# Optimization experiments

Hardware: AMD Instinct MI355X
Metric: run time of the kernel (lower is better)

The kernel has to match this reference:

```python
import jax, jax.numpy as jnp
import numpy as np
from jax import lax

DIM = 512
HEADS = 8
HEAD_DIM = DIM // HEADS
FS = 56            # features_size -> H = W = 56
SR = 2             # sr_ratio
N = FS * FS        # query tokens = 3136
KN = (FS // SR) ** 2  # kv tokens = 784
B = 4
SCALE = HEAD_DIM ** -0.5
LN_EPS = 1e-5


def _relative_indices(fs):
    # matches generate_relative_distance: [[x, y] for x in range(fs) for y in range(fs)]
    coords = np.stack(np.meshgrid(np.arange(fs), np.arange(fs), indexing='ij'), -1).reshape(-1, 2)
    dist = coords[None, :, :] - coords[:, None, :] + (fs - 1)   # (N, N, 2), values in [0, 2fs-2]
    return jnp.asarray(dist, dtype=jnp.int32)


def setup_inputs() -> dict:
    key = jax.random.key(0)
    ks = jax.random.split(key, 8)
    s = 0.02
    return {
        'x':    jax.random.normal(ks[0], (B, DIM, FS, FS), jnp.float32),
        'Wq':   jax.random.normal(ks[1], (DIM, DIM), jnp.float32) * s,
        'Wkv':  jax.random.normal(ks[2], (DIM, 2 * DIM), jnp.float32) * s,
        'Wsr':  jax.random.normal(ks[3], (DIM, DIM, SR, SR), jnp.float32) * s,  # OIHW
        'b_sr': jnp.zeros((DIM,), jnp.float32),
        'gamma': jnp.ones((DIM,), jnp.float32),
        'beta':  jnp.zeros((DIM,), jnp.float32),
        'Wp':   jax.random.normal(ks[4], (DIM, DIM), jnp.float32) * s,
        'bp':   jnp.zeros((DIM,), jnp.float32),
        'pos':  jax.random.normal(ks[5], (2 * FS - 1, 2 * FS - 1), jnp.float32) * 0.2,
        'rel_idx': _relative_indices(FS),
    }


def reference(x, Wq, Wkv, Wsr, b_sr, gamma, beta, Wp, bp, pos, rel_idx):
    b, c, h, w = x.shape
    n = h * w
    xq = x.reshape(b, c, n).transpose(0, 2, 1)                      # B N C
    q = (xq @ Wq).reshape(b, n, HEADS, HEAD_DIM).transpose(0, 2, 1, 3)  # B h N d

    # spatial reduction of k/v: Conv2d(k=SR, s=SR) + LayerNorm
    xr = lax.conv_general_dilated(x, Wsr, (SR, SR), 'VALID',
                                  dimension_numbers=('NCHW', 'OIHW', 'NCHW'))
    xr = xr + b_sr[None, :, None, None]
    kn = xr.shape[2] * xr.shape[3]
    xkv = xr.reshape(b, c, kn).transpose(0, 2, 1)                   # B KN C
    mu = xkv.mean(-1, keepdims=True)
    var = ((xkv - mu) ** 2).mean(-1, keepdims=True)
    xkv = (xkv - mu) * lax.rsqrt(var + LN_EPS) * gamma + beta

    # kv projection; rearrange 'B N (dim h l) -> l B h N dim'
    kv = (xkv @ Wkv).reshape(b, kn, HEAD_DIM, HEADS, 2)
    k = kv[..., 0].transpose(0, 3, 1, 2)                            # B h KN d
    v = kv[..., 1].transpose(0, 3, 1, 2)                            # B h KN d

    attn = jnp.einsum('bhnd,bhmd->bhnm', q, k) * SCALE              # B h N KN
    bias = pos[rel_idx[:, :kn, 0], rel_idx[:, :kn, 1]]              # N KN gathered bias
    attn = jax.nn.softmax(attn + bias, axis=-1)

    out = jnp.einsum('bhnm,bhmd->bhnd', attn, v)                    # B h N d
    out = out.transpose(0, 2, 1, 3).reshape(b, n, c)                # B N C
    out = out @ Wp + bp
    return out.transpose(0, 2, 1).reshape(b, c, h, w)
```

## Files before the change

kernel.cpp:

```cpp
#include <hip/hip_runtime.h>
#include <hip/hip_bf16.h>
#include <cstdint>

constexpr int BATCH = 4;
constexpr int CDIM  = 512;
constexpr int NHEAD = 8;
constexpr int HD    = 64;
constexpr int FSP   = 56;
constexpr int NTOK  = FSP * FSP;
constexpr int KH    = 28;
constexpr int KNTOK = KH * KH;
constexpr float SCALE_ATT = 0.125f;
constexpr int BIAS_LD = 832;

typedef _Float16 f16;
typedef __attribute__((ext_vector_type(8))) _Float16 half8;
typedef __attribute__((ext_vector_type(4))) float  floatx4;

__device__ __forceinline__ void tr64(const float* __restrict__ in,
                                     f16* __restrict__ out, int R, int C,
                                     int r0, int c0, float (*sm)[65], int tid) {
  const int rr = tid >> 2, cs = (tid & 3) * 16;
  const float* src = in + (size_t)(r0 + rr) * C + c0 + cs;
#pragma unroll
  for (int j = 0; j < 16; j += 4) *(float4*)&sm[rr][cs + j] = *(const float4*)&src[j];
  __syncthreads();
  f16* dh = out + (size_t)(c0 + rr) * R + r0 + cs;
  half8 v0, v1;
#pragma unroll
  for (int j = 0; j < 8; ++j) v0[j] = (f16)sm[cs + j][rr];
#pragma unroll
  for (int j = 0; j < 8; ++j) v1[j] = (f16)sm[cs + 8 + j][rr];
  *(half8*)&dh[0] = v0;
  *(half8*)&dh[8] = v1;
}

__global__ __launch_bounds__(256) void k_prep(const float* __restrict__ x,
                                              const float* __restrict__ Wq,
                                              const float* __restrict__ Wkv,
                                              const float* __restrict__ Wp,
                                              const float* __restrict__ Wsr,
                                              const float* __restrict__ pos,
                                              f16* __restrict__ xT,
                                              f16* __restrict__ WqT,
                                              f16* __restrict__ WkvT,
                                              f16* __restrict__ WpT,
                                              f16* __restrict__ WsrP,
                                              float* __restrict__ biasT) {
  __shared__ float sm[64][65];
  const int tid = threadIdx.x;
  int bid = blockIdx.x;
  if (bid < 1568) {
    const int b = bid / 392, r = bid % 392;
    tr64(x + (size_t)b * CDIM * NTOK, xT + (size_t)b * NTOK * CDIM,
         CDIM, NTOK, (r % 8) * 64, (r / 8) * 64, sm, tid);
    return;
  }
  bid -= 1568;
  if (bid < 64)  { tr64(Wq,  WqT,  512, 512,  (bid % 8) * 64, (bid / 8) * 64, sm, tid); return; }
  bid -= 64;
  if (bid < 128) { tr64(Wkv, WkvT, 512, 1024, (bid % 8) * 64, (bid / 8) * 64, sm, tid); return; }
  bid -= 128;
  if (bid < 64)  { tr64(Wp,  WpT,  512, 512,  (bid % 8) * 64, (bid / 8) * 64, sm, tid); return; }
  bid -= 64;
  if (bid < 512) {
    const float* src = Wsr + (size_t)bid * 2048;
    f16* dh = WsrP + (size_t)bid * 2048;
    for (int kp = tid; kp < 2048; kp += 256) {
      const int dd = kp >> 9, c = kp & 511;
      dh[kp] = (f16)src[c * 4 + dd];
    }
    return;
  }
  bid -= 512;
  {
    const int n = bid;
    const int in_ = n / FSP, jn = n % FSP;
    const int cbase = 55 * 111 + 55 - in_ * 111 - jn;
    for (int i = tid; i < BIAS_LD; i += 256) {
      const int jc = i >> 6, w = i & 63, txx = w >> 2, tt = w & 3;
      const int m = jc * 64 + tt * 16 + txx;
      float v = -30000.f;
      if (m < KNTOK) {
        const int im = m / FSP, jm = m % FSP;
        v = pos[cbase + im * 111 + jm];
      }
      biasT[(size_t)n * BIAS_LD + i] = v;
    }
  }
}

struct GemmSmem { f16 A[128 * 32]; f16 B[128 * 32]; };

__device__ __forceinline__ void gl_lds(const f16* g, f16* l) {
  __builtin_amdgcn_global_load_lds(
      (const __attribute__((address_space(1))) void*)g,
      (__attribute__((address_space(3))) void*)l, 16, 0, 0);
}

__device__ __forceinline__ void gemm128(GemmSmem* sm,
    const f16* a0, const f16* a1, const f16* b0, const f16* b1,
    int lane, int wv, int wm, int wn, int quad, int tx,
    floatx4 acc[4][4]) {
  f16* lA0 = sm->A + wv * 1024 + lane * 8;
  f16* lA1 = sm->A + wv * 1024 + 512 + lane * 8;
  f16* lB0 = sm->B + wv * 1024 + lane * 8;
  f16* lB1 = sm->B + wv * 1024 + 512 + lane * 8;
  for (int it = 0; it < 16; ++it) {
    gl_lds(a0 + it * 32, lA0);
    gl_lds(a1 + it * 32, lA1);
    gl_lds(b0 + it * 32, lB0);
    gl_lds(b1 + it * 32, lB1);
    __syncthreads();
    half8 af[4], bf[4];
#pragma unroll
    for (int i = 0; i < 4; ++i)
      af[i] = *(const half8*)&sm->A[(wm * 64 + i * 16 + tx) * 32 + quad * 8];
#pragma unroll
    for (int j = 0; j < 4; ++j)
      bf[j] = *(const half8*)&sm->B[(wn * 64 + j * 16 + tx) * 32 + quad * 8];
#pragma unroll
    for (int j = 0; j < 4; ++j)
#pragma unroll
      for (int i = 0; i < 4; ++i)
        acc[i][j] = __builtin_amdgcn_mfma_f32_16x16x32_f16(af[i], bf[j], acc[i][j], 0, 0, 0);
    __syncthreads();
  }
}

#define GEMM128_PRE()                                                     \
  const int tid = threadIdx.x, lane = tid & 63, wv = tid >> 6;            \
  const int wm = wv & 1, wn = wv >> 1, quad = lane >> 4, tx = lane & 15;  \
  const int lr = lane >> 2, lc = (lane & 3) * 8;                          \
  floatx4 acc[4][4];                                                      \
  _Pragma("unroll") for (int i = 0; i < 4; ++i)                           \
  _Pragma("unroll") for (int j = 0; j < 4; ++j)                           \
      acc[i][j] = (floatx4){0.f, 0.f, 0.f, 0.f};

__global__ __launch_bounds__(256) void k_gemmA(const f16* __restrict__ xT,
                                               const f16* __restrict__ WqT,
                                               f16* __restrict__ Qh,
                                               const f16* __restrict__ WsrP,
                                               float* __restrict__ XRp) {
  __shared__ GemmSmem sm;
  GEMM128_PRE();
  int bid = blockIdx.x;
  if (bid < 400) {
    const int b = bid / 100, t = bid % 100;
    const int m0 = (t >> 2) * 128, n0 = (t & 3) * 128;
    const f16* xb = xT + (size_t)b * NTOK * CDIM;
    const int r0 = wv * 32 + lr, r1 = r0 + 16;
    const f16* a0 = xb + (size_t)min(m0 + r0, NTOK - 1) * CDIM + lc;
    const f16* a1 = xb + (size_t)min(m0 + r1, NTOK - 1) * CDIM + lc;
    const f16* b0 = WqT + (size_t)(n0 + r0) * CDIM + lc;
    const f16* b1 = WqT + (size_t)(n0 + r1) * CDIM + lc;
    gemm128(&sm, a0, a1, b0, b1, lane, wv, wm, wn, quad, tx, acc);
    f16* qhB = Qh + (size_t)b * NTOK * CDIM;
#pragma unroll
    for (int i = 0; i < 4; ++i)
#pragma unroll
      for (int rg = 0; rg < 4; ++rg) {
        const int m = m0 + wm * 64 + i * 16 + quad * 4 + rg;
        if (m >= NTOK) continue;
#pragma unroll
        for (int j = 0; j < 4; ++j)
          qhB[(size_t)m * CDIM + n0 + wn * 64 + j * 16 + tx] = (f16)acc[i][j][rg];
      }
  } else {
    bid -= 400;
    const int bkc = bid / 28, r = bid % 28;
    const int b = bkc >> 2, kc = bkc & 3;
    const int m0 = (r >> 2) * 128, n0 = (r & 3) * 128;
    const f16* xb = xT + (size_t)b * NTOK * CDIM;
    const int r0 = wv * 32 + lr, r1 = r0 + 16;
    int am0 = m0 + r0; if (am0 >= KNTOK) am0 = 0;
    int am1 = m0 + r1; if (am1 >= KNTOK) am1 = 0;
    const int sp0 = 112 * (am0 / KH) + 2 * (am0 % KH) + (kc >> 1) * FSP + (kc & 1);
    const int sp1 = 112 * (am1 / KH) + 2 * (am1 % KH) + (kc >> 1) * FSP + (kc & 1);
    const f16* a0 = xb + (size_t)sp0 * CDIM + lc;
    const f16* a1 = xb + (size_t)sp1 * CDIM + lc;
    const f16* b0 = WsrP + (size_t)(n0 + r0) * 2048 + kc * 512 + lc;
    const f16* b1 = WsrP + (size_t)(n0 + r1) * 2048 + kc * 512 + lc;
    gemm128(&sm, a0, a1, b0, b1, lane, wv, wm, wn, quad, tx, acc);
    float* dst = XRp + (size_t)(kc * BATCH + b) * KNTOK * CDIM;
#pragma unroll
    for (int i = 0; i < 4; ++i)
#pragma unroll
      for (int rg = 0; rg < 4; ++rg) {
        const int m = m0 + wm * 64 + i * 16 + quad * 4 + rg;
        if (m >= KNTOK) continue;
#pragma unroll
        for (int j = 0; j < 4; ++j)
          dst[(size_t)m * CDIM + n0 + wn * 64 + j * 16 + tx] = acc[i][j][rg];
      }
  }
}

__global__ __launch_bounds__(256) void k_ln(const float* __restrict__ XRp,
                                            const float* __restrict__ b_sr,
                                            const float* __restrict__ gamma,
                                            const float* __restrict__ beta,
                                            f16* __restrict__ oh) {
  const int row = blockIdx.x;
  const size_t slab = (size_t)BATCH * KNTOK * CDIM;
  const float* p = XRp + (size_t)row * CDIM;
  const int tid = threadIdx.x;
  const float v0 = p[tid] + p[tid + slab] + p[tid + 2 * slab] + p[tid + 3 * slab]
                 + b_sr[tid];
  const float v1 = p[tid + 256] + p[tid + 256 + slab] + p[tid + 256 + 2 * slab]
                 + p[tid + 256 + 3 * slab] + b_sr[tid + 256];
  float s = v0 + v1;
  float s2 = v0 * v0 + v1 * v1;
#pragma unroll
  for (int mask = 32; mask >= 1; mask >>= 1) {
    s  += __shfl_xor(s, mask, 64);
    s2 += __shfl_xor(s2, mask, 64);
  }
  __shared__ float ws[4], ws2[4];
  const int wid = tid >> 6;
  if ((tid & 63) == 0) { ws[wid] = s; ws2[wid] = s2; }
  __syncthreads();
  const float ts  = ws[0] + ws[1] + ws[2] + ws[3];
  const float ts2 = ws2[0] + ws2[1] + ws2[2] + ws2[3];
  const float mu  = ts * (1.f / CDIM);
  const float var = ts2 * (1.f / CDIM) - mu * mu;
  const float rs  = rsqrtf(var + 1e-5f);
  const size_t base = (size_t)row * CDIM;
  oh[base + tid]       = (f16)((v0 - mu) * rs * gamma[tid] + beta[tid]);
  oh[base + tid + 256] = (f16)((v1 - mu) * rs * gamma[tid + 256] + beta[tid + 256]);
}

__global__ __launch_bounds__(256) void k_kvproj(const f16* __restrict__ XRh,
                                                const f16* __restrict__ WkvT,
                                                f16* __restrict__ Kh,
                                                f16* __restrict__ Vt) {
  __shared__ GemmSmem sm;
  GEMM128_PRE();
  const int bid = blockIdx.x;
  const int b = bid / 56, r = bid % 56;
  const int m0 = (r / 8) * 128, n0 = (r % 8) * 128;
  const f16* ab = XRh + (size_t)b * KNTOK * CDIM;
  const int r0 = wv * 32 + lr, r1 = r0 + 16;
  const f16* a0 = ab + (size_t)min(m0 + r0, KNTOK - 1) * CDIM + lc;
  const f16* a1 = ab + (size_t)min(m0 + r1, KNTOK - 1) * CDIM + lc;
  const f16* b0 = WkvT + (size_t)(n0 + r0) * CDIM + lc;
  const f16* b1 = WkvT + (size_t)(n0 + r1) * CDIM + lc;
  gemm128(&sm, a0, a1, b0, b1, lane, wv, wm, wn, quad, tx, acc);
#pragma unroll
  for (int i = 0; i < 4; ++i)
#pragma unroll
    for (int rg = 0; rg < 4; ++rg) {
      const int m = m0 + wm * 64 + i * 16 + quad * 4 + rg;
      if (m >= KNTOK) continue;
#pragma unroll
      for (int j = 0; j < 4; ++j) {
        const int o2 = n0 + wn * 64 + j * 16 + tx;
        const int d = o2 >> 4, hh = (o2 >> 1) & 7;
        const float v = acc[i][j][rg];
        if (o2 & 1)
          Vt[((size_t)(b * NHEAD + hh) * HD + d) * KNTOK + m] = (f16)v;
        else
          Kh[((size_t)(b * NHEAD + hh) * KNTOK + m) * HD + d] = (f16)v;
      }
    }
}

#define LSTR 72
__global__ __launch_bounds__(256) void k_attn(const f16* __restrict__ Qh,
                                              const f16* __restrict__ Kh,
                                              const f16* __restrict__ Vt,
                                              const float* __restrict__ biasT,
                                              f16* __restrict__ Oh) {
  __shared__ f16 Qhs[128][LSTR], Khs[64][LSTR], Vts[64][LSTR];
  __shared__ f16 Ps[4][32][LSTR];
  const int b = blockIdx.x >> 3, h = blockIdx.x & 7;
  const int n0 = blockIdx.y * 128;
  const int tid = threadIdx.x, lane = tid & 63, wv = tid >> 6;
  const int quad = lane >> 4, tx = lane & 15;
  const int rr = tid >> 2, sg = (tid & 3) * 16;
  const int qr = tid >> 1, qs = (tid & 1) * 32;

  const f16* khB = Kh + (size_t)(b * NHEAD + h) * KNTOK * HD;
  const f16* vtB = Vt + (size_t)(b * NHEAD + h) * HD * KNTOK;

  {
    const int qrow = min(n0 + qr, NTOK - 1);
    const f16* src = Qh + ((size_t)b * NTOK + qrow) * CDIM + h * HD + qs;
    *(half8*)&Qhs[qr][qs]      = *(const half8*)&src[0];
    *(half8*)&Qhs[qr][qs + 8]  = *(const half8*)&src[8];
    *(half8*)&Qhs[qr][qs + 16] = *(const half8*)&src[16];
    *(half8*)&Qhs[qr][qs + 24] = *(const half8*)&src[24];
    const size_t koff = (size_t)rr * HD + sg;
    *(half8*)&Khs[rr][sg]     = *(const half8*)&khB[koff];
    *(half8*)&Khs[rr][sg + 8] = *(const half8*)&khB[koff + 8];
    const size_t voff = (size_t)rr * KNTOK + sg;
    *(half8*)&Vts[rr][sg]     = *(const half8*)&vtB[voff];
    *(half8*)&Vts[rr][sg + 8] = *(const half8*)&vtB[voff + 8];
  }

  size_t bbase[2][4];
#pragma unroll
  for (int i = 0; i < 2; ++i)
#pragma unroll
    for (int rg = 0; rg < 4; ++rg) {
      const int grow = min(n0 + wv * 32 + i * 16 + quad * 4 + rg, NTOK - 1);
      bbase[i][rg] = (size_t)grow * BIAS_LD + tx * 4;
    }

  floatx4 acc_o[2][4];
#pragma unroll
  for (int i = 0; i < 2; ++i)
#pragma unroll
    for (int t = 0; t < 4; ++t) acc_o[i][t] = (floatx4){0.f, 0.f, 0.f, 0.f};
  float l_part[2][4] = {};
  __syncthreads();

  half8 nk0, nk1, nv0, nv1;
  for (int jc = 0; jc < 13; ++jc) {
    if (jc < 12) {
      const int mbn = (jc + 1) * 64;
      const int km = min(mbn + rr, KNTOK - 1);
      const size_t koff = (size_t)km * HD + sg;
      nk0 = *(const half8*)&khB[koff];
      nk1 = *(const half8*)&khB[koff + 8];
      const int vc = min(mbn + sg, KNTOK - 16);
      const size_t voff = (size_t)rr * KNTOK + vc;
      nv0 = *(const half8*)&vtB[voff];
      nv1 = *(const half8*)&vtB[voff + 8];
    }

    floatx4 sc[2][4];
#pragma unroll
    for (int i = 0; i < 2; ++i)
#pragma unroll
      for (int t = 0; t < 4; ++t) sc[i][t] = (floatx4){0.f, 0.f, 0.f, 0.f};
#pragma unroll
    for (int ks = 0; ks < 2; ++ks) {
      const int kk = ks * 32 + quad * 8;
      half8 aq[2];
#pragma unroll
      for (int i = 0; i < 2; ++i)
        aq[i] = *(const half8*)&Qhs[wv * 32 + i * 16 + tx][kk];
#pragma unroll
      for (int t = 0; t < 4; ++t) {
        const half8 bk = *(const half8*)&Khs[t * 16 + tx][kk];
#pragma unroll
        for (int i = 0; i < 2; ++i)
          sc[i][t] = __builtin_amdgcn_mfma_f32_16x16x32_f16(aq[i], bk, sc[i][t], 0, 0, 0);
      }
    }

#pragma unroll
    for (int i = 0; i < 2; ++i)
#pragma unroll
      for (int rg = 0; rg < 4; ++rg) {
        const float4 bb = *(const float4*)&biasT[bbase[i][rg] + jc * 64];
        const float p0 = __expf(fmaf(sc[i][0][rg], SCALE_ATT, bb.x));
        const float p1 = __expf(fmaf(sc[i][1][rg], SCALE_ATT, bb.y));
        const float p2 = __expf(fmaf(sc[i][2][rg], SCALE_ATT, bb.z));
        const float p3 = __expf(fmaf(sc[i][3][rg], SCALE_ATT, bb.w));
        l_part[i][rg] += (p0 + p1) + (p2 + p3);
        const int prow = i * 16 + quad * 4 + rg;
        Ps[wv][prow][0 * 16 + tx] = (f16)p0;
        Ps[wv][prow][1 * 16 + tx] = (f16)p1;
        Ps[wv][prow][2 * 16 + tx] = (f16)p2;
        Ps[wv][prow][3 * 16 + tx] = (f16)p3;
      }

#pragma unroll
    for (int ks = 0; ks < 2; ++ks) {
      const int kk = ks * 32 + quad * 8;
      half8 ap[2];
#pragma unroll
      for (int i = 0; i < 2; ++i)
        ap[i] = *(const half8*)&Ps[wv][i * 16 + tx][kk];
#pragma unroll
      for (int t = 0; t < 4; ++t) {
        const half8 bv = *(const half8*)&Vts[t * 16 + tx][kk];
#pragma unroll
        for (int i = 0; i < 2; ++i)
          acc_o[i][t] = __builtin_amdgcn_mfma_f32_16x16x32_f16(ap[i], bv, acc_o[i][t], 0, 0, 0);
      }
    }
    __syncthreads();
    if (jc < 12) {
      *(half8*)&Khs[rr][sg]     = nk0;
      *(half8*)&Khs[rr][sg + 8] = nk1;
      *(half8*)&Vts[rr][sg]     = nv0;
      *(half8*)&Vts[rr][sg + 8] = nv1;
    }
    __syncthreads();
  }

#pragma unroll
  for (int i = 0; i < 2; ++i)
#pragma unroll
    for (int rg = 0; rg < 4; ++rg) {
      float l = l_part[i][rg];
#pragma unroll
      for (int msk = 1; msk < 16; msk <<= 1) l += __shfl_xor(l, msk, 64);
      const float inv = 1.f / l;
      const int grow = n0 + wv * 32 + i * 16 + quad * 4 + rg;
      if (grow < NTOK) {
        const size_t base = ((size_t)b * NTOK + grow) * CDIM + h * HD;
#pragma unroll
        for (int t = 0; t < 4; ++t)
          Oh[base + t * 16 + tx] = (f16)(acc_o[i][t][rg] * inv);
      }
    }
}

__global__ __launch_bounds__(256) void k_outproj(const f16* __restrict__ Og,
                                                 const f16* __restrict__ WpT,
                                                 const float* __restrict__ bp,
                                                 float* __restrict__ out) {
  __shared__ GemmSmem sm;
  GEMM128_PRE();
  const int bid = blockIdx.x;
  const int b = bid / 100, t = bid % 100;
  const int m0 = (t >> 2) * 128, n0 = (t & 3) * 128;
  const f16* ab = Og + (size_t)b * NTOK * CDIM;
  const int r0 = wv * 32 + lr, r1 = r0 + 16;
  const f16* a0 = ab + (size_t)min(m0 + r0, NTOK - 1) * CDIM + lc;
  const f16* a1 = ab + (size_t)min(m0 + r1, NTOK - 1) * CDIM + lc;
  const f16* b0 = WpT + (size_t)(n0 + r0) * CDIM + lc;
  const f16* b1 = WpT + (size_t)(n0 + r1) * CDIM + lc;
  gemm128(&sm, a0, a1, b0, b1, lane, wv, wm, wn, quad, tx, acc);
#pragma unroll
  for (int j = 0; j < 4; ++j) {
    const int co = n0 + wn * 64 + j * 16 + tx;
    const float bpv = bp[co];
    float* obase = out + ((size_t)b * CDIM + co) * NTOK;
#pragma unroll
    for (int i = 0; i < 4; ++i) {
      const int mb4 = m0 + wm * 64 + i * 16 + quad * 4;
      if (mb4 < NTOK) {
        floatx4 v = acc[i][j] + bpv;
        *(floatx4*)&obase[mb4] = v;
      }
    }
  }
}

extern "C" void kernel_launch(void* const* d_in, const int* in_sizes, int n_in,
                              void* d_out, int out_size, void* d_ws, size_t ws_size,
                              hipStream_t stream) {
  const float* x     = (const float*)d_in[0];
  const float* Wq    = (const float*)d_in[1];
  const float* Wkv   = (const float*)d_in[2];
  const float* Wsr   = (const float*)d_in[3];
  const float* b_sr  = (const float*)d_in[4];
  const float* gamma = (const float*)d_in[5];
  const float* beta  = (const float*)d_in[6];
  const float* Wp    = (const float*)d_in[7];
  const float* bp    = (const float*)d_in[8];
  const float* pos   = (const float*)d_in[9];
  float* out = (float*)d_out;

  char* p = (char*)d_ws;
  auto alloc = [&](size_t bytes) -> void* {
    void* r = (void*)p;
    p += (bytes + 255) & ~(size_t)255;
    return r;
  };
  const size_t SZ_BNC = (size_t)BATCH * NTOK * CDIM;
  const size_t SZ_BKC = (size_t)BATCH * KNTOK * CDIM;
  const size_t SZ_KV  = (size_t)BATCH * NHEAD * KNTOK * HD;

  f16* xT    = (f16*)alloc(SZ_BNC * 2);
  f16* WqT   = (f16*)alloc(512 * 512 * 2);
  f16* WkvT  = (f16*)alloc(1024 * 512 * 2);
  f16* WpT   = (f16*)alloc(512 * 512 * 2);
  f16* WsrP  = (f16*)alloc(512 * 2048 * 2);
  f16* Qh    = (f16*)alloc(SZ_BNC * 2);
  float* XRp = (float*)alloc(SZ_BKC * 4 * 4);
  f16* XRh   = (f16*)alloc(SZ_BKC * 2);
  f16* Vt    = (f16*)alloc(SZ_KV * 2);
  float* biasT = (float*)alloc((size_t)NTOK * BIAS_LD * 4);

  f16* Kh = (f16*)XRp;
  f16* Og = xT;

  const dim3 blk(256);
  k_prep   <<<dim3(5472), blk, 0, stream>>>(x, Wq, Wkv, Wp, Wsr, pos,
                                            xT, WqT, WkvT, WpT, WsrP, biasT);
  k_gemmA  <<<dim3(848),  blk, 0, stream>>>(xT, WqT, Qh, WsrP, XRp);
  k_ln     <<<dim3(BATCH * KNTOK), blk, 0, stream>>>(XRp, b_sr, gamma, beta, XRh);
  k_kvproj <<<dim3(224),  blk, 0, stream>>>(XRh, WkvT, Kh, Vt);
  k_attn   <<<dim3(BATCH * NHEAD, 25), blk, 0, stream>>>(Qh, Kh, Vt, biasT, Og);
  k_outproj<<<dim3(400),  blk, 0, stream>>>(Og, WpT, bp, out);
}
```

Before: 284.6 us.

## Fuse Q projection into attention kernel and halve SR-conv split-K partials

The Q projection GEMM moves out of the standalone GEMM kernel into the attention kernel. Each block computes its 128x64 Q tile from xT and WqT in shared memory before the attention loop, so the Qh buffer round trip through global memory goes away. The SR convolution now runs as its own kernel and accumulates two kernel positions per block, which halves the fp32 partial slabs that LayerNorm must read and sum. In exchange, each attention block repeats part of the Q GEMM work with a small 32-wide K step, and the SR conv launches fewer, longer blocks.

```diff
diff --git a/kernel.cpp b/kernel.cpp
--- a/kernel.cpp
+++ b/kernel.cpp
@@ -137,63 +137,43 @@
   _Pragma("unroll") for (int j = 0; j < 4; ++j)                           \
       acc[i][j] = (floatx4){0.f, 0.f, 0.f, 0.f};
 
-__global__ __launch_bounds__(256) void k_gemmA(const f16* __restrict__ xT,
-                                               const f16* __restrict__ WqT,
-                                               f16* __restrict__ Qh,
-                                               const f16* __restrict__ WsrP,
-                                               float* __restrict__ XRp) {
+__global__ __launch_bounds__(256) void k_srconv(const f16* __restrict__ xT,
+                                                const f16* __restrict__ WsrP,
+                                                float* __restrict__ XRp) {
   __shared__ GemmSmem sm;
   GEMM128_PRE();
-  int bid = blockIdx.x;
-  if (bid < 400) {
-    const int b = bid / 100, t = bid % 100;
-    const int m0 = (t >> 2) * 128, n0 = (t & 3) * 128;
-    const f16* xb = xT + (size_t)b * NTOK * CDIM;
-    const int r0 = wv * 32 + lr, r1 = r0 + 16;
-    const f16* a0 = xb + (size_t)min(m0 + r0, NTOK - 1) * CDIM + lc;
-    const f16* a1 = xb + (size_t)min(m0 + r1, NTOK - 1) * CDIM + lc;
-    const f16* b0 = WqT + (size_t)(n0 + r0) * CDIM + lc;
-    const f16* b1 = WqT + (size_t)(n0 + r1) * CDIM + lc;
-    gemm128(&sm, a0, a1, b0, b1, lane, wv, wm, wn, quad, tx, acc);
-    f16* qhB = Qh + (size_t)b * NTOK * CDIM;
-#pragma unroll
-    for (int i = 0; i < 4; ++i)
-#pragma unroll
-      for (int rg = 0; rg < 4; ++rg) {
-        const int m = m0 + wm * 64 + i * 16 + quad * 4 + rg;
-        if (m >= NTOK) continue;
-#pragma unroll
-        for (int j = 0; j < 4; ++j)
-          qhB[(size_t)m * CDIM + n0 + wn * 64 + j * 16 + tx] = (f16)acc[i][j][rg];
-      }
-  } else {
-    bid -= 400;
-    const int bkc = bid / 28, r = bid % 28;
-    const int b = bkc >> 2, kc = bkc & 3;
-    const int m0 = (r >> 2) * 128, n0 = (r & 3) * 128;
-    const f16* xb = xT + (size_t)b * NTOK * CDIM;
-    const int r0 = wv * 32 + lr, r1 = r0 + 16;
-    int am0 = m0 + r0; if (am0 >= KNTOK) am0 = 0;
-    int am1 = m0 + r1; if (am1 >= KNTOK) am1 = 0;
-    const int sp0 = 112 * (am0 / KH) + 2 * (am0 % KH) + (kc >> 1) * FSP + (kc & 1);
-    const int sp1 = 112 * (am1 / KH) + 2 * (am1 % KH) + (kc >> 1) * FSP + (kc & 1);
+  const int bid = blockIdx.x;
+  const int bkc = bid / 28, r = bid % 28;
+  const int b = bkc >> 1, kc2 = bkc & 1;
+  const int m0 = (r >> 2) * 128, n0 = (r & 3) * 128;
+  const f16* xb = xT + (size_t)b * NTOK * CDIM;
+  const int r0 = wv * 32 + lr, r1 = r0 + 16;
+  int am0 = m0 + r0; if (am0 >= KNTOK) am0 = 0;
+  int am1 = m0 + r1; if (am1 >= KNTOK) am1 = 0;
+  const int base0 = 112 * (am0 / KH) + 2 * (am0 % KH);
+  const int base1 = 112 * (am1 / KH) + 2 * (am1 % KH);
+#pragma unroll
+  for (int dd2 = 0; dd2 < 2; ++dd2) {
+    const int dd = kc2 * 2 + dd2;
+    const int sp0 = base0 + (dd >> 1) * FSP + (dd & 1);
+    const int sp1 = base1 + (dd >> 1) * FSP + (dd & 1);
     const f16* a0 = xb + (size_t)sp0 * CDIM + lc;
     const f16* a1 = xb + (size_t)sp1 * CDIM + lc;
-    const f16* b0 = WsrP + (size_t)(n0 + r0) * 2048 + kc * 512 + lc;
-    const f16* b1 = WsrP + (size_t)(n0 + r1) * 2048 + kc * 512 + lc;
+    const f16* b0 = WsrP + (size_t)(n0 + r0) * 2048 + dd * 512 + lc;
+    const f16* b1 = WsrP + (size_t)(n0 + r1) * 2048 + dd * 512 + lc;
     gemm128(&sm, a0, a1, b0, b1, lane, wv, wm, wn, quad, tx, acc);
-    float* dst = XRp + (size_t)(kc * BATCH + b) * KNTOK * CDIM;
-#pragma unroll
-    for (int i = 0; i < 4; ++i)
-#pragma unroll
-      for (int rg = 0; rg < 4; ++rg) {
-        const int m = m0 + wm * 64 + i * 16 + quad * 4 + rg;
-        if (m >= KNTOK) continue;
-#pragma unroll
-        for (int j = 0; j < 4; ++j)
-          dst[(size_t)m * CDIM + n0 + wn * 64 + j * 16 + tx] = acc[i][j][rg];
-      }
-  }
+  }
+  float* dst = XRp + (size_t)(kc2 * BATCH + b) * KNTOK * CDIM;
+#pragma unroll
+  for (int i = 0; i < 4; ++i)
+#pragma unroll
+    for (int rg = 0; rg < 4; ++rg) {
+      const int m = m0 + wm * 64 + i * 16 + quad * 4 + rg;
+      if (m >= KNTOK) continue;
+#pragma unroll
+      for (int j = 0; j < 4; ++j)
+        dst[(size_t)m * CDIM + n0 + wn * 64 + j * 16 + tx] = acc[i][j][rg];
+    }
 }
 
 __global__ __launch_bounds__(256) void k_ln(const float* __restrict__ XRp,
@@ -205,10 +185,8 @@
   const size_t slab = (size_t)BATCH * KNTOK * CDIM;
   const float* p = XRp + (size_t)row * CDIM;
   const int tid = threadIdx.x;
-  const float v0 = p[tid] + p[tid + slab] + p[tid + 2 * slab] + p[tid + 3 * slab]
-                 + b_sr[tid];
-  const float v1 = p[tid + 256] + p[tid + 256 + slab] + p[tid + 256 + 2 * slab]
-                 + p[tid + 256 + 3 * slab] + b_sr[tid + 256];
+  const float v0 = p[tid] + p[tid + slab] + b_sr[tid];
+  const float v1 = p[tid + 256] + p[tid + 256 + slab] + b_sr[tid + 256];
   float s = v0 + v1;
   float s2 = v0 * v0 + v1 * v1;
 #pragma unroll
@@ -266,7 +244,9 @@
 }
 
 #define LSTR 72
-__global__ __launch_bounds__(256) void k_attn(const f16* __restrict__ Qh,
+#define GSTR 40
+__global__ __launch_bounds__(256) void k_attn(const f16* __restrict__ xT,
+                                              const f16* __restrict__ WqT,
                                               const f16* __restrict__ Kh,
                                               const f16* __restrict__ Vt,
                                               const float* __restrict__ biasT,
@@ -278,18 +258,13 @@
   const int tid = threadIdx.x, lane = tid & 63, wv = tid >> 6;
   const int quad = lane >> 4, tx = lane & 15;
   const int rr = tid >> 2, sg = (tid & 3) * 16;
-  const int qr = tid >> 1, qs = (tid & 1) * 32;
-
+
+  const f16* xb  = xT + (size_t)b * NTOK * CDIM;
+  const f16* wq  = WqT + (size_t)(h * HD) * CDIM;
   const f16* khB = Kh + (size_t)(b * NHEAD + h) * KNTOK * HD;
   const f16* vtB = Vt + (size_t)(b * NHEAD + h) * HD * KNTOK;
 
   {
-    const int qrow = min(n0 + qr, NTOK - 1);
-    const f16* src = Qh + ((size_t)b * NTOK + qrow) * CDIM + h * HD + qs;
-    *(half8*)&Qhs[qr][qs]      = *(const half8*)&src[0];
-    *(half8*)&Qhs[qr][qs + 8]  = *(const half8*)&src[8];
-    *(half8*)&Qhs[qr][qs + 16] = *(const half8*)&src[16];
-    *(half8*)&Qhs[qr][qs + 24] = *(const half8*)&src[24];
     const size_t koff = (size_t)rr * HD + sg;
     *(half8*)&Khs[rr][sg]     = *(const half8*)&khB[koff];
     *(half8*)&Khs[rr][sg + 8] = *(const half8*)&khB[koff + 8];
@@ -298,6 +273,53 @@
     *(half8*)&Vts[rr][sg + 8] = *(const half8*)&vtB[voff + 8];
   }
 
+  {
+    f16* Astage = &Qhs[0][0];
+    f16* Bstage = &Ps[0][0][0];
+    const int ar = tid >> 1, as_ = (tid & 1) * 16;
+    const int br = tid >> 2, bs_ = (tid & 3) * 8;
+    const f16* aP = xb + (size_t)min(n0 + ar, NTOK - 1) * CDIM + as_;
+    const f16* bP = wq + (size_t)br * CDIM + bs_;
+    floatx4 qacc[2][4];
+#pragma unroll
+    for (int i = 0; i < 2; ++i)
+#pragma unroll
+      for (int j = 0; j < 4; ++j) qacc[i][j] = (floatx4){0.f, 0.f, 0.f, 0.f};
+    half8 ra0 = *(const half8*)&aP[0], ra1 = *(const half8*)&aP[8];
+    half8 rb0 = *(const half8*)&bP[0];
+    for (int it = 0; it < 16; ++it) {
+      *(half8*)&Astage[ar * GSTR + as_]     = ra0;
+      *(half8*)&Astage[ar * GSTR + as_ + 8] = ra1;
+      *(half8*)&Bstage[br * GSTR + bs_]     = rb0;
+      __syncthreads();
+      if (it + 1 < 16) {
+        const f16* an = aP + (it + 1) * 32;
+        const f16* bn = bP + (it + 1) * 32;
+        ra0 = *(const half8*)&an[0]; ra1 = *(const half8*)&an[8];
+        rb0 = *(const half8*)&bn[0];
+      }
+      half8 af[2];
+#pragma unroll
+      for (int i = 0; i < 2; ++i)
+        af[i] = *(const half8*)&Astage[(wv * 32 + i * 16 + tx) * GSTR + quad * 8];
+#pragma unroll
+      for (int j = 0; j < 4; ++j) {
+        const half8 bf = *(const half8*)&Bstage[(j * 16 + tx) * GSTR + quad * 8];
+#pragma unroll
+        for (int i = 0; i < 2; ++i)
+          qacc[i][j] = __builtin_amdgcn_mfma_f32_16x16x32_f16(af[i], bf, qacc[i][j], 0, 0, 0);
+      }
+      __syncthreads();
+    }
+#pragma unroll
+    for (int i = 0; i < 2; ++i)
+#pragma unroll
+      for (int j = 0; j < 4; ++j)
+#pragma unroll
+        for (int rg = 0; rg < 4; ++rg)
+          Qhs[wv * 32 + i * 16 + quad * 4 + rg][j * 16 + tx] = (f16)qacc[i][j][rg];
+  }
+
   size_t bbase[2][4];
 #pragma unroll
   for (int i = 0; i < 2; ++i)
@@ -313,7 +335,6 @@
 #pragma unroll
     for (int t = 0; t < 4; ++t) acc_o[i][t] = (floatx4){0.f, 0.f, 0.f, 0.f};
   float l_part[2][4] = {};
-  __syncthreads();
 
   half8 nk0, nk1, nv0, nv1;
   for (int jc = 0; jc < 13; ++jc) {
@@ -472,21 +493,20 @@
   f16* WkvT  = (f16*)alloc(1024 * 512 * 2);
   f16* WpT   = (f16*)alloc(512 * 512 * 2);
   f16* WsrP  = (f16*)alloc(512 * 2048 * 2);
-  f16* Qh    = (f16*)alloc(SZ_BNC * 2);
-  float* XRp = (float*)alloc(SZ_BKC * 4 * 4);
+  float* XRp = (float*)alloc(SZ_BKC * 4 * 2);
   f16* XRh   = (f16*)alloc(SZ_BKC * 2);
   f16* Vt    = (f16*)alloc(SZ_KV * 2);
+  f16* Og    = (f16*)alloc(SZ_BNC * 2);
   float* biasT = (float*)alloc((size_t)NTOK * BIAS_LD * 4);
 
   f16* Kh = (f16*)XRp;
-  f16* Og = xT;
 
   const dim3 blk(256);
   k_prep   <<<dim3(5472), blk, 0, stream>>>(x, Wq, Wkv, Wp, Wsr, pos,
                                             xT, WqT, WkvT, WpT, WsrP, biasT);
-  k_gemmA  <<<dim3(848),  blk, 0, stream>>>(xT, WqT, Qh, WsrP, XRp);
+  k_srconv <<<dim3(224),  blk, 0, stream>>>(xT, WsrP, XRp);
   k_ln     <<<dim3(BATCH * KNTOK), blk, 0, stream>>>(XRp, b_sr, gamma, beta, XRh);
   k_kvproj <<<dim3(224),  blk, 0, stream>>>(XRh, WkvT, Kh, Vt);
-  k_attn   <<<dim3(BATCH * NHEAD, 25), blk, 0, stream>>>(Qh, Kh, Vt, biasT, Og);
+  k_attn   <<<dim3(BATCH * NHEAD, 25), blk, 0, stream>>>(xT, WqT, Kh, Vt, biasT, Og);
   k_outproj<<<dim3(400),  blk, 0, stream>>>(Og, WpT, bp, out);
 }
```

New measurement: 297.0 us. +4.4%, slower.

## Halve conv split-K partials, keep Q fragments in registers, coalesce bias writes

Applied to the files above, without the earlier changes.

The spatial-reduction conv GEMM now runs two of the four kernel taps per block and accumulates them in registers. This halves the fp32 partial buffer and the reads LayerNorm does from it, and cuts the gemmA grid from 848 to 624 blocks. Attention drops the shared Q tile: each wave stages its own Q rows through its P scratch buffer and holds the MFMA fragments in registers, which lowers LDS use and repeated LDS reads. The bias prep loop now reads pos contiguously and scatters the writes. Fewer split-K blocks may reduce parallelism, and keeping Q in registers raises register pressure.

```diff
diff --git a/kernel.cpp b/kernel.cpp
--- a/kernel.cpp
+++ b/kernel.cpp
@@ -77,15 +77,12 @@
     const int n = bid;
     const int in_ = n / FSP, jn = n % FSP;
     const int cbase = 55 * 111 + 55 - in_ * 111 - jn;
-    for (int i = tid; i < BIAS_LD; i += 256) {
-      const int jc = i >> 6, w = i & 63, txx = w >> 2, tt = w & 3;
-      const int m = jc * 64 + tt * 16 + txx;
+    float* dst = biasT + (size_t)n * BIAS_LD;
+    for (int m = tid; m < BIAS_LD; m += 256) {
       float v = -30000.f;
-      if (m < KNTOK) {
-        const int im = m / FSP, jm = m % FSP;
-        v = pos[cbase + im * 111 + jm];
-      }
-      biasT[(size_t)n * BIAS_LD + i] = v;
+      if (m < KNTOK) v = pos[cbase + (m / FSP) * 111 + (m % FSP)];
+      const int jc = m >> 6, w = m & 63, t = w >> 4, txx = w & 15;
+      dst[jc * 64 + txx * 4 + t] = v;
     }
   }
 }
@@ -169,20 +166,26 @@
   } else {
     bid -= 400;
     const int bkc = bid / 28, r = bid % 28;
-    const int b = bkc >> 2, kc = bkc & 3;
+    const int b = bkc >> 1, kc2 = bkc & 1;
     const int m0 = (r >> 2) * 128, n0 = (r & 3) * 128;
     const f16* xb = xT + (size_t)b * NTOK * CDIM;
     const int r0 = wv * 32 + lr, r1 = r0 + 16;
     int am0 = m0 + r0; if (am0 >= KNTOK) am0 = 0;
     int am1 = m0 + r1; if (am1 >= KNTOK) am1 = 0;
-    const int sp0 = 112 * (am0 / KH) + 2 * (am0 % KH) + (kc >> 1) * FSP + (kc & 1);
-    const int sp1 = 112 * (am1 / KH) + 2 * (am1 % KH) + (kc >> 1) * FSP + (kc & 1);
-    const f16* a0 = xb + (size_t)sp0 * CDIM + lc;
-    const f16* a1 = xb + (size_t)sp1 * CDIM + lc;
-    const f16* b0 = WsrP + (size_t)(n0 + r0) * 2048 + kc * 512 + lc;
-    const f16* b1 = WsrP + (size_t)(n0 + r1) * 2048 + kc * 512 + lc;
-    gemm128(&sm, a0, a1, b0, b1, lane, wv, wm, wn, quad, tx, acc);
-    float* dst = XRp + (size_t)(kc * BATCH + b) * KNTOK * CDIM;
+    const int base0 = 112 * (am0 / KH) + 2 * (am0 % KH);
+    const int base1 = 112 * (am1 / KH) + 2 * (am1 % KH);
+#pragma unroll
+    for (int dd2 = 0; dd2 < 2; ++dd2) {
+      const int dd = kc2 * 2 + dd2;
+      const int sp0 = base0 + (dd >> 1) * FSP + (dd & 1);
+      const int sp1 = base1 + (dd >> 1) * FSP + (dd & 1);
+      const f16* a0 = xb + (size_t)sp0 * CDIM + lc;
+      const f16* a1 = xb + (size_t)sp1 * CDIM + lc;
+      const f16* b0 = WsrP + (size_t)(n0 + r0) * 2048 + dd * 512 + lc;
+      const f16* b1 = WsrP + (size_t)(n0 + r1) * 2048 + dd * 512 + lc;
+      gemm128(&sm, a0, a1, b0, b1, lane, wv, wm, wn, quad, tx, acc);
+    }
+    float* dst = XRp + (size_t)(kc2 * BATCH + b) * KNTOK * CDIM;
 #pragma unroll
     for (int i = 0; i < 4; ++i)
 #pragma unroll
@@ -205,10 +208,8 @@
   const size_t slab = (size_t)BATCH * KNTOK * CDIM;
   const float* p = XRp + (size_t)row * CDIM;
   const int tid = threadIdx.x;
-  const float v0 = p[tid] + p[tid + slab] + p[tid + 2 * slab] + p[tid + 3 * slab]
-                 + b_sr[tid];
-  const float v1 = p[tid + 256] + p[tid + 256 + slab] + p[tid + 256 + 2 * slab]
-                 + p[tid + 256 + 3 * slab] + b_sr[tid + 256];
+  const float v0 = p[tid] + p[tid + slab] + b_sr[tid];
+  const float v1 = p[tid + 256] + p[tid + 256 + slab] + b_sr[tid + 256];
   float s = v0 + v1;
   float s2 = v0 * v0 + v1 * v1;
 #pragma unroll
@@ -271,31 +272,41 @@
                                               const f16* __restrict__ Vt,
                                               const float* __restrict__ biasT,
                                               f16* __restrict__ Oh) {
-  __shared__ f16 Qhs[128][LSTR], Khs[64][LSTR], Vts[64][LSTR];
+  __shared__ f16 Khs[64][LSTR], Vts[64][LSTR];
   __shared__ f16 Ps[4][32][LSTR];
   const int b = blockIdx.x >> 3, h = blockIdx.x & 7;
   const int n0 = blockIdx.y * 128;
   const int tid = threadIdx.x, lane = tid & 63, wv = tid >> 6;
   const int quad = lane >> 4, tx = lane & 15;
   const int rr = tid >> 2, sg = (tid & 3) * 16;
-  const int qr = tid >> 1, qs = (tid & 1) * 32;
 
   const f16* khB = Kh + (size_t)(b * NHEAD + h) * KNTOK * HD;
   const f16* vtB = Vt + (size_t)(b * NHEAD + h) * HD * KNTOK;
+  f16* PsW = &Ps[wv][0][0];
 
   {
-    const int qrow = min(n0 + qr, NTOK - 1);
-    const f16* src = Qh + ((size_t)b * NTOK + qrow) * CDIM + h * HD + qs;
-    *(half8*)&Qhs[qr][qs]      = *(const half8*)&src[0];
-    *(half8*)&Qhs[qr][qs + 8]  = *(const half8*)&src[8];
-    *(half8*)&Qhs[qr][qs + 16] = *(const half8*)&src[16];
-    *(half8*)&Qhs[qr][qs + 24] = *(const half8*)&src[24];
     const size_t koff = (size_t)rr * HD + sg;
     *(half8*)&Khs[rr][sg]     = *(const half8*)&khB[koff];
     *(half8*)&Khs[rr][sg + 8] = *(const half8*)&khB[koff + 8];
     const size_t voff = (size_t)rr * KNTOK + sg;
     *(half8*)&Vts[rr][sg]     = *(const half8*)&vtB[voff];
     *(half8*)&Vts[rr][sg + 8] = *(const half8*)&vtB[voff + 8];
+  }
+
+  half8 qreg[2][2];
+  {
+    const int qr2 = lane >> 1, qs2 = (lane & 1) * 32;
+    const int qrow = min(n0 + wv * 32 + qr2, NTOK - 1);
+    const f16* src = Qh + ((size_t)b * NTOK + qrow) * CDIM + h * HD + qs2;
+    *(half8*)&PsW[qr2 * LSTR + qs2]      = *(const half8*)&src[0];
+    *(half8*)&PsW[qr2 * LSTR + qs2 + 8]  = *(const half8*)&src[8];
+    *(half8*)&PsW[qr2 * LSTR + qs2 + 16] = *(const half8*)&src[16];
+    *(half8*)&PsW[qr2 * LSTR + qs2 + 24] = *(const half8*)&src[24];
+#pragma unroll
+    for (int i = 0; i < 2; ++i)
+#pragma unroll
+      for (int ks = 0; ks < 2; ++ks)
+        qreg[i][ks] = *(const half8*)&PsW[(i * 16 + tx) * LSTR + ks * 32 + quad * 8];
   }
 
   size_t bbase[2][4];
@@ -337,16 +348,12 @@
 #pragma unroll
     for (int ks = 0; ks < 2; ++ks) {
       const int kk = ks * 32 + quad * 8;
-      half8 aq[2];
-#pragma unroll
-      for (int i = 0; i < 2; ++i)
-        aq[i] = *(const half8*)&Qhs[wv * 32 + i * 16 + tx][kk];
 #pragma unroll
       for (int t = 0; t < 4; ++t) {
         const half8 bk = *(const half8*)&Khs[t * 16 + tx][kk];
 #pragma unroll
         for (int i = 0; i < 2; ++i)
-          sc[i][t] = __builtin_amdgcn_mfma_f32_16x16x32_f16(aq[i], bk, sc[i][t], 0, 0, 0);
+          sc[i][t] = __builtin_amdgcn_mfma_f32_16x16x32_f16(qreg[i][ks], bk, sc[i][t], 0, 0, 0);
       }
     }
 
@@ -361,10 +368,10 @@
         const float p3 = __expf(fmaf(sc[i][3][rg], SCALE_ATT, bb.w));
         l_part[i][rg] += (p0 + p1) + (p2 + p3);
         const int prow = i * 16 + quad * 4 + rg;
-        Ps[wv][prow][0 * 16 + tx] = (f16)p0;
-        Ps[wv][prow][1 * 16 + tx] = (f16)p1;
-        Ps[wv][prow][2 * 16 + tx] = (f16)p2;
-        Ps[wv][prow][3 * 16 + tx] = (f16)p3;
+        PsW[prow * LSTR + 0 * 16 + tx] = (f16)p0;
+        PsW[prow * LSTR + 1 * 16 + tx] = (f16)p1;
+        PsW[prow * LSTR + 2 * 16 + tx] = (f16)p2;
+        PsW[prow * LSTR + 3 * 16 + tx] = (f16)p3;
       }
 
 #pragma unroll
@@ -373,7 +380,7 @@
       half8 ap[2];
 #pragma unroll
       for (int i = 0; i < 2; ++i)
-        ap[i] = *(const half8*)&Ps[wv][i * 16 + tx][kk];
+        ap[i] = *(const half8*)&PsW[(i * 16 + tx) * LSTR + kk];
 #pragma unroll
       for (int t = 0; t < 4; ++t) {
         const half8 bv = *(const half8*)&Vts[t * 16 + tx][kk];
@@ -473,7 +480,7 @@
   f16* WpT   = (f16*)alloc(512 * 512 * 2);
   f16* WsrP  = (f16*)alloc(512 * 2048 * 2);
   f16* Qh    = (f16*)alloc(SZ_BNC * 2);
-  float* XRp = (float*)alloc(SZ_BKC * 4 * 4);
+  float* XRp = (float*)alloc(SZ_BKC * 4 * 2);
   f16* XRh   = (f16*)alloc(SZ_BKC * 2);
   f16* Vt    = (f16*)alloc(SZ_KV * 2);
   float* biasT = (float*)alloc((size_t)NTOK * BIAS_LD * 4);
@@ -484,7 +491,7 @@
   const dim3 blk(256);
   k_prep   <<<dim3(5472), blk, 0, stream>>>(x, Wq, Wkv, Wp, Wsr, pos,
                                             xT, WqT, WkvT, WpT, WsrP, biasT);
-  k_gemmA  <<<dim3(848),  blk, 0, stream>>>(xT, WqT, Qh, WsrP, XRp);
+  k_gemmA  <<<dim3(624),  blk, 0, stream>>>(xT, WqT, Qh, WsrP, XRp);
   k_ln     <<<dim3(BATCH * KNTOK), blk, 0, stream>>>(XRp, b_sr, gamma, beta, XRh);
   k_kvproj <<<dim3(224),  blk, 0, stream>>>(XRh, WkvT, Kh, Vt);
   k_attn   <<<dim3(BATCH * NHEAD, 25), blk, 0, stream>>>(Qh, Kh, Vt, biasT, Og);
```

Result: slower. 327.5 us (+15.1%).

## Move Wkv/Wp transposes and bias table build into the GEMM-A launch

Applied to the files above, without the earlier changes.

The Wkv and Wp transposes and the relative-position bias table construction move out of the prep kernel and run as extra blocks of the Q/spatial-reduction GEMM launch, since only later kernels need them. The idea is to shrink the serial prep kernel and let that independent work fill idle CUs during the GEMM phase. Shared memory becomes a union arena sized for the transpose tile. The bias write pattern is also restructured so global reads of pos are sequential and the permutation happens on the store side, which may make the stores less coalesced.

```diff
diff --git a/kernel.cpp b/kernel.cpp
--- a/kernel.cpp
+++ b/kernel.cpp
@@ -37,16 +37,10 @@
 
 __global__ __launch_bounds__(256) void k_prep(const float* __restrict__ x,
                                               const float* __restrict__ Wq,
-                                              const float* __restrict__ Wkv,
-                                              const float* __restrict__ Wp,
                                               const float* __restrict__ Wsr,
-                                              const float* __restrict__ pos,
                                               f16* __restrict__ xT,
                                               f16* __restrict__ WqT,
-                                              f16* __restrict__ WkvT,
-                                              f16* __restrict__ WpT,
-                                              f16* __restrict__ WsrP,
-                                              float* __restrict__ biasT) {
+                                              f16* __restrict__ WsrP) {
   __shared__ float sm[64][65];
   const int tid = threadIdx.x;
   int bid = blockIdx.x;
@@ -57,35 +51,14 @@
     return;
   }
   bid -= 1568;
-  if (bid < 64)  { tr64(Wq,  WqT,  512, 512,  (bid % 8) * 64, (bid / 8) * 64, sm, tid); return; }
+  if (bid < 64) { tr64(Wq, WqT, 512, 512, (bid % 8) * 64, (bid / 8) * 64, sm, tid); return; }
   bid -= 64;
-  if (bid < 128) { tr64(Wkv, WkvT, 512, 1024, (bid % 8) * 64, (bid / 8) * 64, sm, tid); return; }
-  bid -= 128;
-  if (bid < 64)  { tr64(Wp,  WpT,  512, 512,  (bid % 8) * 64, (bid / 8) * 64, sm, tid); return; }
-  bid -= 64;
-  if (bid < 512) {
+  {
     const float* src = Wsr + (size_t)bid * 2048;
     f16* dh = WsrP + (size_t)bid * 2048;
     for (int kp = tid; kp < 2048; kp += 256) {
       const int dd = kp >> 9, c = kp & 511;
       dh[kp] = (f16)src[c * 4 + dd];
-    }
-    return;
-  }
-  bid -= 512;
-  {
-    const int n = bid;
-    const int in_ = n / FSP, jn = n % FSP;
-    const int cbase = 55 * 111 + 55 - in_ * 111 - jn;
-    for (int i = tid; i < BIAS_LD; i += 256) {
-      const int jc = i >> 6, w = i & 63, txx = w >> 2, tt = w & 3;
-      const int m = jc * 64 + tt * 16 + txx;
-      float v = -30000.f;
-      if (m < KNTOK) {
-        const int im = m / FSP, jm = m % FSP;
-        v = pos[cbase + im * 111 + jm];
-      }
-      biasT[(size_t)n * BIAS_LD + i] = v;
     }
   }
 }
@@ -128,8 +101,8 @@
   }
 }
 
-#define GEMM128_PRE()                                                     \
-  const int tid = threadIdx.x, lane = tid & 63, wv = tid >> 6;            \
+#define GEMM128_VARS()                                                    \
+  const int lane = tid & 63, wv = tid >> 6;                               \
   const int wm = wv & 1, wn = wv >> 1, quad = lane >> 4, tx = lane & 15;  \
   const int lr = lane >> 2, lc = (lane & 3) * 8;                          \
   floatx4 acc[4][4];                                                      \
@@ -141,58 +114,87 @@
                                                const f16* __restrict__ WqT,
                                                f16* __restrict__ Qh,
                                                const f16* __restrict__ WsrP,
-                                               float* __restrict__ XRp) {
-  __shared__ GemmSmem sm;
-  GEMM128_PRE();
+                                               float* __restrict__ XRp,
+                                               const float* __restrict__ Wkv,
+                                               const float* __restrict__ Wp,
+                                               const float* __restrict__ pos,
+                                               f16* __restrict__ WkvT,
+                                               f16* __restrict__ WpT,
+                                               float* __restrict__ biasT) {
+  __shared__ __align__(16) char arena[64 * 65 * 4];
+  GemmSmem* sm = (GemmSmem*)arena;
+  float (*tsm)[65] = (float(*)[65])arena;
+  const int tid = threadIdx.x;
   int bid = blockIdx.x;
-  if (bid < 400) {
-    const int b = bid / 100, t = bid % 100;
-    const int m0 = (t >> 2) * 128, n0 = (t & 3) * 128;
-    const f16* xb = xT + (size_t)b * NTOK * CDIM;
-    const int r0 = wv * 32 + lr, r1 = r0 + 16;
-    const f16* a0 = xb + (size_t)min(m0 + r0, NTOK - 1) * CDIM + lc;
-    const f16* a1 = xb + (size_t)min(m0 + r1, NTOK - 1) * CDIM + lc;
-    const f16* b0 = WqT + (size_t)(n0 + r0) * CDIM + lc;
-    const f16* b1 = WqT + (size_t)(n0 + r1) * CDIM + lc;
-    gemm128(&sm, a0, a1, b0, b1, lane, wv, wm, wn, quad, tx, acc);
-    f16* qhB = Qh + (size_t)b * NTOK * CDIM;
-#pragma unroll
-    for (int i = 0; i < 4; ++i)
-#pragma unroll
-      for (int rg = 0; rg < 4; ++rg) {
-        const int m = m0 + wm * 64 + i * 16 + quad * 4 + rg;
-        if (m >= NTOK) continue;
-#pragma unroll
-        for (int j = 0; j < 4; ++j)
-          qhB[(size_t)m * CDIM + n0 + wn * 64 + j * 16 + tx] = (f16)acc[i][j][rg];
-      }
-  } else {
-    bid -= 400;
-    const int bkc = bid / 28, r = bid % 28;
-    const int b = bkc >> 2, kc = bkc & 3;
-    const int m0 = (r >> 2) * 128, n0 = (r & 3) * 128;
-    const f16* xb = xT + (size_t)b * NTOK * CDIM;
-    const int r0 = wv * 32 + lr, r1 = r0 + 16;
-    int am0 = m0 + r0; if (am0 >= KNTOK) am0 = 0;
-    int am1 = m0 + r1; if (am1 >= KNTOK) am1 = 0;
-    const int sp0 = 112 * (am0 / KH) + 2 * (am0 % KH) + (kc >> 1) * FSP + (kc & 1);
-    const int sp1 = 112 * (am1 / KH) + 2 * (am1 % KH) + (kc >> 1) * FSP + (kc & 1);
-    const f16* a0 = xb + (size_t)sp0 * CDIM + lc;
-    const f16* a1 = xb + (size_t)sp1 * CDIM + lc;
-    const f16* b0 = WsrP + (size_t)(n0 + r0) * 2048 + kc * 512 + lc;
-    const f16* b1 = WsrP + (size_t)(n0 + r1) * 2048 + kc * 512 + lc;
-    gemm128(&sm, a0, a1, b0, b1, lane, wv, wm, wn, quad, tx, acc);
-    float* dst = XRp + (size_t)(kc * BATCH + b) * KNTOK * CDIM;
-#pragma unroll
-    for (int i = 0; i < 4; ++i)
-#pragma unroll
-      for (int rg = 0; rg < 4; ++rg) {
-        const int m = m0 + wm * 64 + i * 16 + quad * 4 + rg;
-        if (m >= KNTOK) continue;
-#pragma unroll
-        for (int j = 0; j < 4; ++j)
-          dst[(size_t)m * CDIM + n0 + wn * 64 + j * 16 + tx] = acc[i][j][rg];
-      }
+  if (bid < 848) {
+    GEMM128_VARS();
+    if (bid < 400) {
+      const int b = bid / 100, t = bid % 100;
+      const int m0 = (t >> 2) * 128, n0 = (t & 3) * 128;
+      const f16* xb = xT + (size_t)b * NTOK * CDIM;
+      const int r0 = wv * 32 + lr, r1 = r0 + 16;
+      const f16* a0 = xb + (size_t)min(m0 + r0, NTOK - 1) * CDIM + lc;
+      const f16* a1 = xb + (size_t)min(m0 + r1, NTOK - 1) * CDIM + lc;
+      const f16* b0 = WqT + (size_t)(n0 + r0) * CDIM + lc;
+      const f16* b1 = WqT + (size_t)(n0 + r1) * CDIM + lc;
+      gemm128(sm, a0, a1, b0, b1, lane, wv, wm, wn, quad, tx, acc);
+      f16* qhB = Qh + (size_t)b * NTOK * CDIM;
+#pragma unroll
+      for (int i = 0; i < 4; ++i)
+#pragma unroll
+        for (int rg = 0; rg < 4; ++rg) {
+          const int m = m0 + wm * 64 + i * 16 + quad * 4 + rg;
+          if (m >= NTOK) continue;
+#pragma unroll
+          for (int j = 0; j < 4; ++j)
+            qhB[(size_t)m * CDIM + n0 + wn * 64 + j * 16 + tx] = (f16)acc[i][j][rg];
+        }
+    } else {
+      bid -= 400;
+      const int bkc = bid / 28, r = bid % 28;
+      const int b = bkc >> 2, kc = bkc & 3;
+      const int m0 = (r >> 2) * 128, n0 = (r & 3) * 128;
+      const f16* xb = xT + (size_t)b * NTOK * CDIM;
+      const int r0 = wv * 32 + lr, r1 = r0 + 16;
+      int am0 = m0 + r0; if (am0 >= KNTOK) am0 = 0;
+      int am1 = m0 + r1; if (am1 >= KNTOK) am1 = 0;
+      const int sp0 = 112 * (am0 / KH) + 2 * (am0 % KH) + (kc >> 1) * FSP + (kc & 1);
+      const int sp1 = 112 * (am1 / KH) + 2 * (am1 % KH) + (kc >> 1) * FSP + (kc & 1);
+      const f16* a0 = xb + (size_t)sp0 * CDIM + lc;
+      const f16* a1 = xb + (size_t)sp1 * CDIM + lc;
+      const f16* b0 = WsrP + (size_t)(n0 + r0) * 2048 + kc * 512 + lc;
+      const f16* b1 = WsrP + (size_t)(n0 + r1) * 2048 + kc * 512 + lc;
+      gemm128(sm, a0, a1, b0, b1, lane, wv, wm, wn, quad, tx, acc);
+      float* dst = XRp + (size_t)(kc * BATCH + b) * KNTOK * CDIM;
+#pragma unroll
+      for (int i = 0; i < 4; ++i)
+#pragma unroll
+        for (int rg = 0; rg < 4; ++rg) {
+          const int m = m0 + wm * 64 + i * 16 + quad * 4 + rg;
+          if (m >= KNTOK) continue;
+#pragma unroll
+          for (int j = 0; j < 4; ++j)
+            dst[(size_t)m * CDIM + n0 + wn * 64 + j * 16 + tx] = acc[i][j][rg];
+        }
+    }
+    return;
+  }
+  bid -= 848;
+  if (bid < 128) { tr64(Wkv, WkvT, 512, 1024, (bid % 8) * 64, (bid / 8) * 64, tsm, tid); return; }
+  bid -= 128;
+  if (bid < 64)  { tr64(Wp,  WpT,  512, 512,  (bid % 8) * 64, (bid / 8) * 64, tsm, tid); return; }
+  bid -= 64;
+  {
+    const int n = bid;
+    const int in_ = n / FSP, jn = n % FSP;
+    const int cbase = 55 * 111 + 55 - in_ * 111 - jn;
+    float* dst = biasT + (size_t)n * BIAS_LD;
+    for (int m = tid; m < BIAS_LD; m += 256) {
+      float v = -30000.f;
+      if (m < KNTOK) v = pos[cbase + (m / FSP) * 111 + (m % FSP)];
+      const int jc = m >> 6, w = m & 63, t = w >> 4, txx = w & 15;
+      dst[jc * 64 + txx * 4 + t] = v;
+    }
   }
 }
 
@@ -234,8 +236,10 @@
                                                 const f16* __restrict__ WkvT,
                                                 f16* __restrict__ Kh,
                                                 f16* __restrict__ Vt) {
-  __shared__ GemmSmem sm;
-  GEMM128_PRE();
+  __shared__ GemmSmem smem;
+  GemmSmem* sm = &smem;
+  const int tid = threadIdx.x;
+  GEMM128_VARS();
   const int bid = blockIdx.x;
   const int b = bid / 56, r = bid % 56;
   const int m0 = (r / 8) * 128, n0 = (r % 8) * 128;
@@ -245,7 +249,7 @@
   const f16* a1 = ab + (size_t)min(m0 + r1, KNTOK - 1) * CDIM + lc;
   const f16* b0 = WkvT + (size_t)(n0 + r0) * CDIM + lc;
   const f16* b1 = WkvT + (size_t)(n0 + r1) * CDIM + lc;
-  gemm128(&sm, a0, a1, b0, b1, lane, wv, wm, wn, quad, tx, acc);
+  gemm128(sm, a0, a1, b0, b1, lane, wv, wm, wn, quad, tx, acc);
 #pragma unroll
   for (int i = 0; i < 4; ++i)
 #pragma unroll
@@ -414,8 +418,10 @@
                                                  const f16* __restrict__ WpT,
                                                  const float* __restrict__ bp,
                                                  float* __restrict__ out) {
-  __shared__ GemmSmem sm;
-  GEMM128_PRE();
+  __shared__ GemmSmem smem;
+  GemmSmem* sm = &smem;
+  const int tid = threadIdx.x;
+  GEMM128_VARS();
   const int bid = blockIdx.x;
   const int b = bid / 100, t = bid % 100;
   const int m0 = (t >> 2) * 128, n0 = (t & 3) * 128;
@@ -425,7 +431,7 @@
   const f16* a1 = ab + (size_t)min(m0 + r1, NTOK - 1) * CDIM + lc;
   const f16* b0 = WpT + (size_t)(n0 + r0) * CDIM + lc;
   const f16* b1 = WpT + (size_t)(n0 + r1) * CDIM + lc;
-  gemm128(&sm, a0, a1, b0, b1, lane, wv, wm, wn, quad, tx, acc);
+  gemm128(sm, a0, a1, b0, b1, lane, wv, wm, wn, quad, tx, acc);
 #pragma unroll
   for (int j = 0; j < 4; ++j) {
     const int co = n0 + wn * 64 + j * 16 + tx;
@@ -482,9 +488,9 @@
   f16* Og = xT;
 
   const dim3 blk(256);
-  k_prep   <<<dim3(5472), blk, 0, stream>>>(x, Wq, Wkv, Wp, Wsr, pos,
-                                            xT, WqT, WkvT, WpT, WsrP, biasT);
-  k_gemmA  <<<dim3(848),  blk, 0, stream>>>(xT, WqT, Qh, WsrP, XRp);
+  k_prep   <<<dim3(2144), blk, 0, stream>>>(x, Wq, Wsr, xT, WqT, WsrP);
+  k_gemmA  <<<dim3(4176), blk, 0, stream>>>(xT, WqT, Qh, WsrP, XRp,
+                                            Wkv, Wp, pos, WkvT, WpT, biasT);
   k_ln     <<<dim3(BATCH * KNTOK), blk, 0, stream>>>(XRp, b_sr, gamma, beta, XRh);
   k_kvproj <<<dim3(224),  blk, 0, stream>>>(XRh, WkvT, Kh, Vt);
   k_attn   <<<dim3(BATCH * NHEAD, 25), blk, 0, stream>>>(Qh, Kh, Vt, biasT, Og);
```

New measurement: 287.5 us. About the same (+1.0%).
